# Performance work log

Hardware: AMD Instinct MI355X
Metric: run time of the kernel (lower is better)

The kernel has to match this reference:

```python
import jax, jax.numpy as jnp
import numpy as np

INV_SQRT2 = np.float32(2.0 ** -0.5)
EPS = 1e-5


def _bn5(x, g, b, m, v):
    # inference-mode BatchNorm3d over channel axis 1 of NCDHW
    r = (1, -1, 1, 1, 1)
    return (x - m.reshape(r)) * (g.reshape(r) * jax.lax.rsqrt(v.reshape(r) + EPS)) + b.reshape(r)


def _conv3d(x, w, b, dil=1, pad=0):
    out = jax.lax.conv_general_dilated(
        x, w, window_strides=(1, 1, 1), padding=[(pad, pad)] * 3,
        rhs_dilation=(dil, dil, dil),
        dimension_numbers=('NCDHW', 'OIDHW', 'NCDHW'))
    return out + b.reshape(1, -1, 1, 1, 1)


def _haar_dwt2(x):
    # pywt dwt2(x, 'haar', axes=(-3,-2)) for even-length axes.
    # axis -3 (D): a = approx, d = detail (pywt sign: (x0 - x1)/sqrt2)
    a = (x[:, :, 0::2] + x[:, :, 1::2]) * INV_SQRT2
    d = (x[:, :, 0::2] - x[:, :, 1::2]) * INV_SQRT2
    # axis -2 (H)
    LL = (a[:, :, :, 0::2] + a[:, :, :, 1::2]) * INV_SQRT2  # 'aa'
    HL = (a[:, :, :, 0::2] - a[:, :, :, 1::2]) * INV_SQRT2  # 'ad'
    LH = (d[:, :, :, 0::2] + d[:, :, :, 1::2]) * INV_SQRT2  # 'da'
    HH = (d[:, :, :, 0::2] - d[:, :, :, 1::2]) * INV_SQRT2  # 'dd'
    return LL, LH, HL, HH


def setup_inputs() -> dict:
    key = jax.random.key(0)
    ks = jax.random.split(key, 12)
    B, C1, D, H, W = 2, 60, 128, 128, 64
    CH, R = 64, 4  # gate channels, CH // reduction_ratio
    f32 = jnp.float32
    inp = {
        'x1': jax.random.normal(ks[0], (B, C1, D // 2, H // 2, W), f32),
        'x2': jax.random.normal(ks[1], (B, 1, D, H, W), f32),
        # BatchNorm3d(4) on dwt features
        'bn_g': jnp.ones(4, f32), 'bn_b': jnp.zeros(4, f32),
        'bn_m': jnp.zeros(4, f32), 'bn_v': jnp.ones(4, f32),
        # BAM channel gate: Linear(64->4), BN1d(4), Linear(4->64)
        'cg_w1': jax.random.normal(ks[2], (R, CH), f32) * 0.05,
        'cg_b1': jnp.zeros(R, f32),
        'cg_bng': jnp.ones(R, f32), 'cg_bnb': jnp.zeros(R, f32),
        'cg_bnm': jnp.zeros(R, f32), 'cg_bnv': jnp.ones(R, f32),
        'cg_w2': jax.random.normal(ks[3], (CH, R), f32) * 0.05,
        'cg_b2': jnp.zeros(CH, f32),
        # BAM spatial gate
        'sg_w0': jax.random.normal(ks[4], (R, CH, 1, 1, 1), f32) * 0.05,
        'sg_b0': jnp.zeros(R, f32),
        'sg_g0': jnp.ones(R, f32), 'sg_be0': jnp.zeros(R, f32),
        'sg_m0': jnp.zeros(R, f32), 'sg_v0': jnp.ones(R, f32),
        'sg_w1': jax.random.normal(ks[5], (R, R, 3, 3, 3), f32) * 0.05,
        'sg_b1': jnp.zeros(R, f32),
        'sg_g1': jnp.ones(R, f32), 'sg_be1': jnp.zeros(R, f32),
        'sg_m1': jnp.zeros(R, f32), 'sg_v1': jnp.ones(R, f32),
        'sg_w2': jax.random.normal(ks[6], (R, R, 3, 3, 3), f32) * 0.05,
        'sg_b2': jnp.zeros(R, f32),
        'sg_g2': jnp.ones(R, f32), 'sg_be2': jnp.zeros(R, f32),
        'sg_m2': jnp.zeros(R, f32), 'sg_v2': jnp.ones(R, f32),
        'sg_w3': jax.random.normal(ks[7], (1, R, 1, 1, 1), f32) * 0.05,
        'sg_b3': jnp.zeros(1, f32),
    }
    return inp


def reference(x1, x2, bn_g, bn_b, bn_m, bn_v,
              cg_w1, cg_b1, cg_bng, cg_bnb, cg_bnm, cg_bnv, cg_w2, cg_b2,
              sg_w0, sg_b0, sg_g0, sg_be0, sg_m0, sg_v0,
              sg_w1, sg_b1, sg_g1, sg_be1, sg_m1, sg_v1,
              sg_w2, sg_b2, sg_g2, sg_be2, sg_m2, sg_v2,
              sg_w3, sg_b3):
    LL, LH, HL, HH = _haar_dwt2(x2)
    dwt = jnp.concatenate([LL, LH, HL, HH], axis=1)          # [B,4,D/2,H/2,W]
    dwt = jax.nn.relu(_bn5(dwt, bn_g, bn_b, bn_m, bn_v))
    feat = jnp.concatenate([dwt, x1], axis=1)                # [B,64,D/2,H/2,W]

    # BAM channel gate
    pooled = feat.mean(axis=(2, 3, 4))                        # [B,64]
    h = pooled @ cg_w1.T + cg_b1
    h = jax.nn.relu((h - cg_bnm) * (cg_bng * jax.lax.rsqrt(cg_bnv + EPS)) + cg_bnb)
    att_c = (h @ cg_w2.T + cg_b2)[:, :, None, None, None]     # [B,64,1,1,1]

    # BAM spatial gate
    s = jax.nn.relu(_bn5(_conv3d(feat, sg_w0, sg_b0), sg_g0, sg_be0, sg_m0, sg_v0))
    s = jax.nn.relu(_bn5(_conv3d(s, sg_w1, sg_b1, dil=4, pad=4), sg_g1, sg_be1, sg_m1, sg_v1))
    s = jax.nn.relu(_bn5(_conv3d(s, sg_w2, sg_b2, dil=4, pad=4), sg_g2, sg_be2, sg_m2, sg_v2))
    att_s = _conv3d(s, sg_w3, sg_b3)                          # [B,1,D/2,H/2,W]

    scale = 1.0 + jax.nn.sigmoid(att_c + att_s)
    return (feat * scale, LL)
```

## Files before the change

### kernel.cpp

```cpp
#include <hip/hip_runtime.h>
#include <math.h>

#define EPSBN 1e-5f

constexpr int B   = 2;
constexpr int C1  = 60;
constexpr int NV  = 64 * 64 * 64;
constexpr int NB  = NV / 1024;

__global__ __launch_bounds__(256) void kA(
    const float* __restrict__ x1, const float* __restrict__ x2,
    const float* __restrict__ bn_g, const float* __restrict__ bn_b,
    const float* __restrict__ bn_m, const float* __restrict__ bn_v,
    const float* __restrict__ sg_w0, const float* __restrict__ sg_b0,
    const float* __restrict__ sg_g0, const float* __restrict__ sg_be0,
    const float* __restrict__ sg_m0, const float* __restrict__ sg_v0,
    float* __restrict__ dwt, float* __restrict__ s0,
    float* __restrict__ part, float* __restrict__ outLL)
{
    __shared__ float w0l[256];
    __shared__ float cA[4], cB[4];
    __shared__ float dsc[4], dsh[4];
    __shared__ float wsum[64][4];

    const int tid = threadIdx.x;
    w0l[tid] = sg_w0[tid];
    if (tid < 4) {
        float sc = sg_g0[tid] * rsqrtf(sg_v0[tid] + EPSBN);
        cA[tid] = sc;
        cB[tid] = (sg_b0[tid] - sg_m0[tid]) * sc + sg_be0[tid];
        float d = bn_g[tid] * rsqrtf(bn_v[tid] + EPSBN);
        dsc[tid] = d;
        dsh[tid] = bn_b[tid] - bn_m[tid] * d;
    }
    __syncthreads();

    const int b = blockIdx.y;
    const int v = blockIdx.x * 1024 + tid * 4;
    const int x = v & 63, y = (v >> 6) & 63, z = v >> 12;
    const int lane = tid & 63, wv = tid >> 6;

    const float* px2 = x2 + (size_t)b * (128 * 128 * 64);
    const size_t i00 = ((size_t)(2 * z) * 128 + 2 * y) * 64 + x;
    const float4 p00 = *(const float4*)(px2 + i00);
    const float4 p01 = *(const float4*)(px2 + i00 + 64);
    const float4 p10 = *(const float4*)(px2 + i00 + 8192);
    const float4 p11 = *(const float4*)(px2 + i00 + 8256);
    const float* q00 = (const float*)&p00; const float* q01 = (const float*)&p01;
    const float* q10 = (const float*)&p10; const float* q11 = (const float*)&p11;

    float tv[4][4];
    float llv[4];
    #pragma unroll
    for (int vi = 0; vi < 4; ++vi) {
        float a = q00[vi], bb = q01[vi], c = q10[vi], d = q11[vi];
        float LL = 0.5f * (a + bb + c + d);
        float LH = 0.5f * (a + bb - c - d);
        float HL = 0.5f * (a - bb + c - d);
        float HH = 0.5f * (a - bb - c + d);
        llv[vi] = LL;
        tv[vi][0] = fmaxf(LL * dsc[0] + dsh[0], 0.f);
        tv[vi][1] = fmaxf(LH * dsc[1] + dsh[1], 0.f);
        tv[vi][2] = fmaxf(HL * dsc[2] + dsh[2], 0.f);
        tv[vi][3] = fmaxf(HH * dsc[3] + dsh[3], 0.f);
    }
    *(float4*)(outLL + (size_t)b * NV + v) = make_float4(llv[0], llv[1], llv[2], llv[3]);

    float acc[4][4] = {};
    #pragma unroll
    for (int c = 0; c < 4; ++c) {
        #pragma unroll
        for (int vi = 0; vi < 4; ++vi) {
            float t = tv[vi][c];
            #pragma unroll
            for (int r = 0; r < 4; ++r) acc[vi][r] += w0l[r * 64 + c] * t;
        }
        float rs = tv[0][c] + tv[1][c] + tv[2][c] + tv[3][c];
        #pragma unroll
        for (int off = 32; off; off >>= 1) rs += __shfl_xor(rs, off);
        if (lane == 0) wsum[c][wv] = rs;
    }

    float4* pdwt = (float4*)dwt + (size_t)b * NV + v;
    #pragma unroll
    for (int vi = 0; vi < 4; ++vi)
        pdwt[vi] = make_float4(tv[vi][0], tv[vi][1], tv[vi][2], tv[vi][3]);

    const float* px1 = x1 + (size_t)b * C1 * NV + v;
    for (int c = 0; c < C1; ++c) {
        const float4 f = *(const float4*)(px1 + (size_t)c * NV);
        const float* fv = (const float*)&f;
        #pragma unroll
        for (int vi = 0; vi < 4; ++vi) {
            #pragma unroll
            for (int r = 0; r < 4; ++r) acc[vi][r] += w0l[r * 64 + 4 + c] * fv[vi];
        }
        float rs = f.x + f.y + f.z + f.w;
        #pragma unroll
        for (int off = 32; off; off >>= 1) rs += __shfl_xor(rs, off);
        if (lane == 0) wsum[4 + c][wv] = rs;
    }

    float4* ps0 = (float4*)s0 + (size_t)b * NV + v;
    #pragma unroll
    for (int vi = 0; vi < 4; ++vi)
        ps0[vi] = make_float4(fmaxf(acc[vi][0] * cA[0] + cB[0], 0.f),
                              fmaxf(acc[vi][1] * cA[1] + cB[1], 0.f),
                              fmaxf(acc[vi][2] * cA[2] + cB[2], 0.f),
                              fmaxf(acc[vi][3] * cA[3] + cB[3], 0.f));

    __syncthreads();
    if (tid < 64) {
        float p = wsum[tid][0] + wsum[tid][1] + wsum[tid][2] + wsum[tid][3];
        part[((size_t)b * 64 + tid) * NB + blockIdx.x] = p;
    }
}

__global__ __launch_bounds__(256) void kConv1(
    const float* __restrict__ sin_,
    const float* __restrict__ w, const float* __restrict__ bias,
    const float* __restrict__ g, const float* __restrict__ be,
    const float* __restrict__ m, const float* __restrict__ vv,
    float* __restrict__ outp)
{
    __shared__ float wl[432];
    __shared__ float cA[4], cB[4];
    const int tid = threadIdx.x;
    for (int i = tid; i < 432; i += 256) wl[i] = w[i];
    if (tid < 4) {
        float sc = g[tid] * rsqrtf(vv[tid] + EPSBN);
        cA[tid] = sc;
        cB[tid] = (bias[tid] - m[tid]) * sc + be[tid];
    }
    __syncthreads();

    const int b = blockIdx.y;
    const int v = blockIdx.x * 1024 + tid * 4;
    const int x = v & 63, y = (v >> 6) & 63, z = v >> 12;
    const float4* pin = (const float4*)sin_ + (size_t)b * NV;

    float acc[4][4] = {};
    #pragma unroll
    for (int kz = -1; kz <= 1; ++kz) {
        const int zz = z + 4 * kz;
        if ((unsigned)zz >= 64u) continue;
        #pragma unroll
        for (int ky = -1; ky <= 1; ++ky) {
            const int yy = y + 4 * ky;
            if ((unsigned)yy >= 64u) continue;
            #pragma unroll
            for (int kx = -1; kx <= 1; ++kx) {
                const int xx = x + 4 * kx;
                if ((unsigned)xx >= 64u) continue;
                const int t = (kz + 1) * 9 + (ky + 1) * 3 + (kx + 1);
                const int vt = zz * 4096 + yy * 64 + xx;
                #pragma unroll
                for (int vi = 0; vi < 4; ++vi) {
                    const float4 tap = pin[vt + vi];
                    acc[vi][0] += wl[      t] * tap.x + wl[ 27 + t] * tap.y + wl[ 54 + t] * tap.z + wl[ 81 + t] * tap.w;
                    acc[vi][1] += wl[108 + t] * tap.x + wl[135 + t] * tap.y + wl[162 + t] * tap.z + wl[189 + t] * tap.w;
                    acc[vi][2] += wl[216 + t] * tap.x + wl[243 + t] * tap.y + wl[270 + t] * tap.z + wl[297 + t] * tap.w;
                    acc[vi][3] += wl[324 + t] * tap.x + wl[351 + t] * tap.y + wl[378 + t] * tap.z + wl[405 + t] * tap.w;
                }
            }
        }
    }

    float4* po = (float4*)outp + (size_t)b * NV + v;
    #pragma unroll
    for (int vi = 0; vi < 4; ++vi)
        po[vi] = make_float4(fmaxf(acc[vi][0] * cA[0] + cB[0], 0.f),
                             fmaxf(acc[vi][1] * cA[1] + cB[1], 0.f),
                             fmaxf(acc[vi][2] * cA[2] + cB[2], 0.f),
                             fmaxf(acc[vi][3] * cA[3] + cB[3], 0.f));
}

__global__ __launch_bounds__(256) void kMLP(
    const float* __restrict__ part,
    const float* __restrict__ cg_w1, const float* __restrict__ cg_b1,
    const float* __restrict__ cg_bng, const float* __restrict__ cg_bnb,
    const float* __restrict__ cg_bnm, const float* __restrict__ cg_bnv,
    const float* __restrict__ cg_w2, const float* __restrict__ cg_b2,
    float* __restrict__ att_c)
{
    const int b = blockIdx.x;
    const int tid = threadIdx.x;
    __shared__ float pooled[64];
    __shared__ float h[4];

    const int c = tid >> 2, q = tid & 3;
    const float4* pp = (const float4*)(part + ((size_t)b * 64 + c) * NB + q * 64);
    float sm = 0.f;
    #pragma unroll
    for (int i = 0; i < 16; ++i) { float4 f = pp[i]; sm += f.x + f.y + f.z + f.w; }
    sm += __shfl_xor(sm, 1);
    sm += __shfl_xor(sm, 2);
    if (q == 0) pooled[c] = sm * (1.0f / NV);
    __syncthreads();
    if (tid < 4) {
        float a = cg_b1[tid];
        for (int cc = 0; cc < 64; ++cc) a += pooled[cc] * cg_w1[tid * 64 + cc];
        float sc = cg_bng[tid] * rsqrtf(cg_bnv[tid] + EPSBN);
        h[tid] = fmaxf((a - cg_bnm[tid]) * sc + cg_bnb[tid], 0.f);
    }
    __syncthreads();
    if (tid < 64) {
        float a = cg_b2[tid];
        #pragma unroll
        for (int r = 0; r < 4; ++r) a += h[r] * cg_w2[tid * 4 + r];
        att_c[b * 64 + tid] = a;
    }
}

__global__ __launch_bounds__(256) void kF(
    const float* __restrict__ x1,
    const float* __restrict__ dwt,
    const float* __restrict__ s1,
    const float* __restrict__ w, const float* __restrict__ bias,
    const float* __restrict__ g, const float* __restrict__ be,
    const float* __restrict__ m, const float* __restrict__ vv,
    const float* __restrict__ w3, const float* __restrict__ b3,
    const float* __restrict__ att_c,
    float* __restrict__ out0)
{
    __shared__ float wl[432];
    __shared__ float cA[4], cB[4], w3l[4], b3l;
    __shared__ float ec[64];
    const int tid = threadIdx.x;
    const int b = blockIdx.y;
    for (int i = tid; i < 432; i += 256) wl[i] = w[i];
    if (tid < 4) {
        float sc = g[tid] * rsqrtf(vv[tid] + EPSBN);
        cA[tid] = sc;
        cB[tid] = (bias[tid] - m[tid]) * sc + be[tid];
        w3l[tid] = w3[tid];
    }
    if (tid == 0) b3l = b3[0];
    if (tid < 64) ec[tid] = __expf(-att_c[b * 64 + tid]);
    __syncthreads();

    const int v = blockIdx.x * 1024 + tid * 4;
    const int x = v & 63, y = (v >> 6) & 63, z = v >> 12;
    const float4* pin = (const float4*)s1 + (size_t)b * NV;

    float acc[4][4] = {};
    #pragma unroll
    for (int kz = -1; kz <= 1; ++kz) {
        const int zz = z + 4 * kz;
        if ((unsigned)zz >= 64u) continue;
        #pragma unroll
        for (int ky = -1; ky <= 1; ++ky) {
            const int yy = y + 4 * ky;
            if ((unsigned)yy >= 64u) continue;
            #pragma unroll
            for (int kx = -1; kx <= 1; ++kx) {
                const int xx = x + 4 * kx;
                if ((unsigned)xx >= 64u) continue;
                const int t = (kz + 1) * 9 + (ky + 1) * 3 + (kx + 1);
                const int vt = zz * 4096 + yy * 64 + xx;
                #pragma unroll
                for (int vi = 0; vi < 4; ++vi) {
                    const float4 tap = pin[vt + vi];
                    acc[vi][0] += wl[      t] * tap.x + wl[ 27 + t] * tap.y + wl[ 54 + t] * tap.z + wl[ 81 + t] * tap.w;
                    acc[vi][1] += wl[108 + t] * tap.x + wl[135 + t] * tap.y + wl[162 + t] * tap.z + wl[189 + t] * tap.w;
                    acc[vi][2] += wl[216 + t] * tap.x + wl[243 + t] * tap.y + wl[270 + t] * tap.z + wl[297 + t] * tap.w;
                    acc[vi][3] += wl[324 + t] * tap.x + wl[351 + t] * tap.y + wl[378 + t] * tap.z + wl[405 + t] * tap.w;
                }
            }
        }
    }

    float eas[4];
    #pragma unroll
    for (int vi = 0; vi < 4; ++vi) {
        float r0 = fmaxf(acc[vi][0] * cA[0] + cB[0], 0.f);
        float r1 = fmaxf(acc[vi][1] * cA[1] + cB[1], 0.f);
        float r2 = fmaxf(acc[vi][2] * cA[2] + cB[2], 0.f);
        float r3 = fmaxf(acc[vi][3] * cA[3] + cB[3], 0.f);
        float as = b3l + w3l[0] * r0 + w3l[1] * r1 + w3l[2] * r2 + w3l[3] * r3;
        eas[vi] = __expf(-as);
    }

    float dv[4][4];
    const float4* pdwt = (const float4*)dwt + (size_t)b * NV + v;
    #pragma unroll
    for (int vi = 0; vi < 4; ++vi) {
        const float4 dq = pdwt[vi];
        dv[vi][0] = dq.x; dv[vi][1] = dq.y; dv[vi][2] = dq.z; dv[vi][3] = dq.w;
    }
    float* po = out0 + (size_t)b * 64 * NV + v;
    #pragma unroll
    for (int c = 0; c < 4; ++c) {
        float e = ec[c];
        float4 o;
        o.x = dv[0][c] * (1.f + __builtin_amdgcn_rcpf(1.f + e * eas[0]));
        o.y = dv[1][c] * (1.f + __builtin_amdgcn_rcpf(1.f + e * eas[1]));
        o.z = dv[2][c] * (1.f + __builtin_amdgcn_rcpf(1.f + e * eas[2]));
        o.w = dv[3][c] * (1.f + __builtin_amdgcn_rcpf(1.f + e * eas[3]));
        *(float4*)(po + (size_t)c * NV) = o;
    }
    const float* px1 = x1 + (size_t)b * C1 * NV + v;
    for (int c = 0; c < C1; ++c) {
        const float4 f = *(const float4*)(px1 + (size_t)c * NV);
        const float e = ec[4 + c];
        float4 o;
        o.x = f.x * (1.f + __builtin_amdgcn_rcpf(1.f + e * eas[0]));
        o.y = f.y * (1.f + __builtin_amdgcn_rcpf(1.f + e * eas[1]));
        o.z = f.z * (1.f + __builtin_amdgcn_rcpf(1.f + e * eas[2]));
        o.w = f.w * (1.f + __builtin_amdgcn_rcpf(1.f + e * eas[3]));
        *(float4*)(po + (size_t)(4 + c) * NV) = o;
    }
}

extern "C" void kernel_launch(void* const* d_in, const int* in_sizes, int n_in,
                              void* d_out, int out_size, void* d_ws, size_t ws_size,
                              hipStream_t stream)
{
    const float* x1 = (const float*)d_in[0];
    const float* x2 = (const float*)d_in[1];
    const float* bn_g = (const float*)d_in[2];
    const float* bn_b = (const float*)d_in[3];
    const float* bn_m = (const float*)d_in[4];
    const float* bn_v = (const float*)d_in[5];
    const float* cg_w1 = (const float*)d_in[6];
    const float* cg_b1 = (const float*)d_in[7];
    const float* cg_bng = (const float*)d_in[8];
    const float* cg_bnb = (const float*)d_in[9];
    const float* cg_bnm = (const float*)d_in[10];
    const float* cg_bnv = (const float*)d_in[11];
    const float* cg_w2 = (const float*)d_in[12];
    const float* cg_b2 = (const float*)d_in[13];
    const float* sg_w0 = (const float*)d_in[14];
    const float* sg_b0 = (const float*)d_in[15];
    const float* sg_g0 = (const float*)d_in[16];
    const float* sg_be0 = (const float*)d_in[17];
    const float* sg_m0 = (const float*)d_in[18];
    const float* sg_v0 = (const float*)d_in[19];
    const float* sg_w1 = (const float*)d_in[20];
    const float* sg_b1 = (const float*)d_in[21];
    const float* sg_g1 = (const float*)d_in[22];
    const float* sg_be1 = (const float*)d_in[23];
    const float* sg_m1 = (const float*)d_in[24];
    const float* sg_v1 = (const float*)d_in[25];
    const float* sg_w2 = (const float*)d_in[26];
    const float* sg_b2 = (const float*)d_in[27];
    const float* sg_g2 = (const float*)d_in[28];
    const float* sg_be2 = (const float*)d_in[29];
    const float* sg_m2 = (const float*)d_in[30];
    const float* sg_v2 = (const float*)d_in[31];
    const float* sg_w3 = (const float*)d_in[32];
    const float* sg_b3 = (const float*)d_in[33];

    float* ws = (float*)d_ws;
    float* dwt  = ws;
    float* s0   = ws + 2097152;
    float* s1   = ws + 4194304;
    float* part = ws + 6291456;
    float* attc = ws + 6324224;

    float* out0  = (float*)d_out;
    float* outLL = out0 + (size_t)B * 64 * NV;

    dim3 grid(NB, B), blk(256);
    kA<<<grid, blk, 0, stream>>>(x1, x2, bn_g, bn_b, bn_m, bn_v,
                                 sg_w0, sg_b0, sg_g0, sg_be0, sg_m0, sg_v0,
                                 dwt, s0, part, outLL);
    kConv1<<<grid, blk, 0, stream>>>(s0, sg_w1, sg_b1, sg_g1, sg_be1, sg_m1, sg_v1, s1);
    kMLP<<<dim3(B), blk, 0, stream>>>(part, cg_w1, cg_b1, cg_bng, cg_bnb, cg_bnm, cg_bnv,
                                      cg_w2, cg_b2, attc);
    kF<<<grid, blk, 0, stream>>>(x1, dwt, s1, sg_w2, sg_b2, sg_g2, sg_be2, sg_m2, sg_v2,
                                 sg_w3, sg_b3, attc, out0);
}
```

Measured before the change: 120.7 us.

## Halve per-thread work, fold channel MLP into conv1, split final gating into streaming kernel

Each thread now handles 2 voxels instead of 4, which doubles the grid of the stencil and pointwise kernels. The channel-gate MLP moves into an extra block of the first dilated conv, removing a separate launch. The dwt intermediate is stored channel-major. The last conv now writes a per-voxel exp(-att_s) map, and a new flat, fully coalesced multiply kernel applies the gate over all 64 channels. This aims for more parallelism and better-coalesced streaming in the final pass, at the cost of an extra round trip of the spatial-attention map through memory and one more launch.

```diff
diff --git a/kernel.cpp b/kernel.cpp
--- a/kernel.cpp
+++ b/kernel.cpp
@@ -6,7 +6,7 @@
 constexpr int B   = 2;
 constexpr int C1  = 60;
 constexpr int NV  = 64 * 64 * 64;
-constexpr int NB  = NV / 1024;
+constexpr int NBa = NV / 512;
 
 __global__ __launch_bounds__(256) void kA(
     const float* __restrict__ x1, const float* __restrict__ x2,
@@ -15,7 +15,7 @@
     const float* __restrict__ sg_w0, const float* __restrict__ sg_b0,
     const float* __restrict__ sg_g0, const float* __restrict__ sg_be0,
     const float* __restrict__ sg_m0, const float* __restrict__ sg_v0,
-    float* __restrict__ dwt, float* __restrict__ s0,
+    float* __restrict__ dwtM, float* __restrict__ s0,
     float* __restrict__ part, float* __restrict__ outLL)
 {
     __shared__ float w0l[256];
@@ -36,23 +36,22 @@
     __syncthreads();
 
     const int b = blockIdx.y;
-    const int v = blockIdx.x * 1024 + tid * 4;
+    const int v = blockIdx.x * 512 + tid * 2;
     const int x = v & 63, y = (v >> 6) & 63, z = v >> 12;
     const int lane = tid & 63, wv = tid >> 6;
 
     const float* px2 = x2 + (size_t)b * (128 * 128 * 64);
     const size_t i00 = ((size_t)(2 * z) * 128 + 2 * y) * 64 + x;
-    const float4 p00 = *(const float4*)(px2 + i00);
-    const float4 p01 = *(const float4*)(px2 + i00 + 64);
-    const float4 p10 = *(const float4*)(px2 + i00 + 8192);
-    const float4 p11 = *(const float4*)(px2 + i00 + 8256);
+    const float2 p00 = *(const float2*)(px2 + i00);
+    const float2 p01 = *(const float2*)(px2 + i00 + 64);
+    const float2 p10 = *(const float2*)(px2 + i00 + 8192);
+    const float2 p11 = *(const float2*)(px2 + i00 + 8256);
     const float* q00 = (const float*)&p00; const float* q01 = (const float*)&p01;
     const float* q10 = (const float*)&p10; const float* q11 = (const float*)&p11;
 
-    float tv[4][4];
-    float llv[4];
-    #pragma unroll
-    for (int vi = 0; vi < 4; ++vi) {
+    float tv[2][4], llv[2];
+    #pragma unroll
+    for (int vi = 0; vi < 2; ++vi) {
         float a = q00[vi], bb = q01[vi], c = q10[vi], d = q11[vi];
         float LL = 0.5f * (a + bb + c + d);
         float LH = 0.5f * (a + bb - c - d);
@@ -64,38 +63,33 @@
         tv[vi][2] = fmaxf(HL * dsc[2] + dsh[2], 0.f);
         tv[vi][3] = fmaxf(HH * dsc[3] + dsh[3], 0.f);
     }
-    *(float4*)(outLL + (size_t)b * NV + v) = make_float4(llv[0], llv[1], llv[2], llv[3]);
-
-    float acc[4][4] = {};
+    *(float2*)(outLL + (size_t)b * NV + v) = make_float2(llv[0], llv[1]);
+
+    float acc[2][4] = {};
     #pragma unroll
     for (int c = 0; c < 4; ++c) {
         #pragma unroll
-        for (int vi = 0; vi < 4; ++vi) {
+        for (int vi = 0; vi < 2; ++vi) {
             float t = tv[vi][c];
             #pragma unroll
             for (int r = 0; r < 4; ++r) acc[vi][r] += w0l[r * 64 + c] * t;
         }
-        float rs = tv[0][c] + tv[1][c] + tv[2][c] + tv[3][c];
+        float rs = tv[0][c] + tv[1][c];
         #pragma unroll
         for (int off = 32; off; off >>= 1) rs += __shfl_xor(rs, off);
         if (lane == 0) wsum[c][wv] = rs;
-    }
-
-    float4* pdwt = (float4*)dwt + (size_t)b * NV + v;
-    #pragma unroll
-    for (int vi = 0; vi < 4; ++vi)
-        pdwt[vi] = make_float4(tv[vi][0], tv[vi][1], tv[vi][2], tv[vi][3]);
+        *(float2*)(dwtM + ((size_t)b * 4 + c) * NV + v) = make_float2(tv[0][c], tv[1][c]);
+    }
 
     const float* px1 = x1 + (size_t)b * C1 * NV + v;
     for (int c = 0; c < C1; ++c) {
-        const float4 f = *(const float4*)(px1 + (size_t)c * NV);
-        const float* fv = (const float*)&f;
-        #pragma unroll
-        for (int vi = 0; vi < 4; ++vi) {
-            #pragma unroll
-            for (int r = 0; r < 4; ++r) acc[vi][r] += w0l[r * 64 + 4 + c] * fv[vi];
-        }
-        float rs = f.x + f.y + f.z + f.w;
+        const float2 f = *(const float2*)(px1 + (size_t)c * NV);
+        #pragma unroll
+        for (int r = 0; r < 4; ++r) {
+            acc[0][r] += w0l[r * 64 + 4 + c] * f.x;
+            acc[1][r] += w0l[r * 64 + 4 + c] * f.y;
+        }
+        float rs = f.x + f.y;
         #pragma unroll
         for (int off = 32; off; off >>= 1) rs += __shfl_xor(rs, off);
         if (lane == 0) wsum[4 + c][wv] = rs;
@@ -103,7 +97,7 @@
 
     float4* ps0 = (float4*)s0 + (size_t)b * NV + v;
     #pragma unroll
-    for (int vi = 0; vi < 4; ++vi)
+    for (int vi = 0; vi < 2; ++vi)
         ps0[vi] = make_float4(fmaxf(acc[vi][0] * cA[0] + cB[0], 0.f),
                               fmaxf(acc[vi][1] * cA[1] + cB[1], 0.f),
                               fmaxf(acc[vi][2] * cA[2] + cB[2], 0.f),
@@ -112,7 +106,7 @@
     __syncthreads();
     if (tid < 64) {
         float p = wsum[tid][0] + wsum[tid][1] + wsum[tid][2] + wsum[tid][3];
-        part[((size_t)b * 64 + tid) * NB + blockIdx.x] = p;
+        part[((size_t)b * 64 + tid) * NBa + blockIdx.x] = p;
     }
 }
 
@@ -121,11 +115,47 @@
     const float* __restrict__ w, const float* __restrict__ bias,
     const float* __restrict__ g, const float* __restrict__ be,
     const float* __restrict__ m, const float* __restrict__ vv,
+    const float* __restrict__ part,
+    const float* __restrict__ cg_w1, const float* __restrict__ cg_b1,
+    const float* __restrict__ cg_bng, const float* __restrict__ cg_bnb,
+    const float* __restrict__ cg_bnm, const float* __restrict__ cg_bnv,
+    const float* __restrict__ cg_w2, const float* __restrict__ cg_b2,
+    float* __restrict__ ec,
     float* __restrict__ outp)
 {
+    const int tid = threadIdx.x;
+    const int b = blockIdx.y;
+
+    if (blockIdx.x == NBa) {
+        __shared__ float pooled[64];
+        __shared__ float h[4];
+        const int c = tid >> 2, q = tid & 3;
+        const float4* pp = (const float4*)(part + ((size_t)b * 64 + c) * NBa + q * 128);
+        float sm = 0.f;
+        #pragma unroll
+        for (int i = 0; i < 32; ++i) { float4 f = pp[i]; sm += f.x + f.y + f.z + f.w; }
+        sm += __shfl_xor(sm, 1);
+        sm += __shfl_xor(sm, 2);
+        if (q == 0) pooled[c] = sm * (1.0f / NV);
+        __syncthreads();
+        if (tid < 4) {
+            float a = cg_b1[tid];
+            for (int cc = 0; cc < 64; ++cc) a += pooled[cc] * cg_w1[tid * 64 + cc];
+            float sc = cg_bng[tid] * rsqrtf(cg_bnv[tid] + EPSBN);
+            h[tid] = fmaxf((a - cg_bnm[tid]) * sc + cg_bnb[tid], 0.f);
+        }
+        __syncthreads();
+        if (tid < 64) {
+            float a = cg_b2[tid];
+            #pragma unroll
+            for (int r = 0; r < 4; ++r) a += h[r] * cg_w2[tid * 4 + r];
+            ec[b * 64 + tid] = __expf(-a);
+        }
+        return;
+    }
+
     __shared__ float wl[432];
     __shared__ float cA[4], cB[4];
-    const int tid = threadIdx.x;
     for (int i = tid; i < 432; i += 256) wl[i] = w[i];
     if (tid < 4) {
         float sc = g[tid] * rsqrtf(vv[tid] + EPSBN);
@@ -134,12 +164,11 @@
     }
     __syncthreads();
 
-    const int b = blockIdx.y;
-    const int v = blockIdx.x * 1024 + tid * 4;
+    const int v = blockIdx.x * 512 + tid * 2;
     const int x = v & 63, y = (v >> 6) & 63, z = v >> 12;
     const float4* pin = (const float4*)sin_ + (size_t)b * NV;
 
-    float acc[4][4] = {};
+    float acc[2][4] = {};
     #pragma unroll
     for (int kz = -1; kz <= 1; ++kz) {
         const int zz = z + 4 * kz;
@@ -155,7 +184,7 @@
                 const int t = (kz + 1) * 9 + (ky + 1) * 3 + (kx + 1);
                 const int vt = zz * 4096 + yy * 64 + xx;
                 #pragma unroll
-                for (int vi = 0; vi < 4; ++vi) {
+                for (int vi = 0; vi < 2; ++vi) {
                     const float4 tap = pin[vt + vi];
                     acc[vi][0] += wl[      t] * tap.x + wl[ 27 + t] * tap.y + wl[ 54 + t] * tap.z + wl[ 81 + t] * tap.w;
                     acc[vi][1] += wl[108 + t] * tap.x + wl[135 + t] * tap.y + wl[162 + t] * tap.z + wl[189 + t] * tap.w;
@@ -168,66 +197,24 @@
 
     float4* po = (float4*)outp + (size_t)b * NV + v;
     #pragma unroll
-    for (int vi = 0; vi < 4; ++vi)
+    for (int vi = 0; vi < 2; ++vi)
         po[vi] = make_float4(fmaxf(acc[vi][0] * cA[0] + cB[0], 0.f),
                              fmaxf(acc[vi][1] * cA[1] + cB[1], 0.f),
                              fmaxf(acc[vi][2] * cA[2] + cB[2], 0.f),
                              fmaxf(acc[vi][3] * cA[3] + cB[3], 0.f));
 }
 
-__global__ __launch_bounds__(256) void kMLP(
-    const float* __restrict__ part,
-    const float* __restrict__ cg_w1, const float* __restrict__ cg_b1,
-    const float* __restrict__ cg_bng, const float* __restrict__ cg_bnb,
-    const float* __restrict__ cg_bnm, const float* __restrict__ cg_bnv,
-    const float* __restrict__ cg_w2, const float* __restrict__ cg_b2,
-    float* __restrict__ att_c)
-{
-    const int b = blockIdx.x;
-    const int tid = threadIdx.x;
-    __shared__ float pooled[64];
-    __shared__ float h[4];
-
-    const int c = tid >> 2, q = tid & 3;
-    const float4* pp = (const float4*)(part + ((size_t)b * 64 + c) * NB + q * 64);
-    float sm = 0.f;
-    #pragma unroll
-    for (int i = 0; i < 16; ++i) { float4 f = pp[i]; sm += f.x + f.y + f.z + f.w; }
-    sm += __shfl_xor(sm, 1);
-    sm += __shfl_xor(sm, 2);
-    if (q == 0) pooled[c] = sm * (1.0f / NV);
-    __syncthreads();
-    if (tid < 4) {
-        float a = cg_b1[tid];
-        for (int cc = 0; cc < 64; ++cc) a += pooled[cc] * cg_w1[tid * 64 + cc];
-        float sc = cg_bng[tid] * rsqrtf(cg_bnv[tid] + EPSBN);
-        h[tid] = fmaxf((a - cg_bnm[tid]) * sc + cg_bnb[tid], 0.f);
-    }
-    __syncthreads();
-    if (tid < 64) {
-        float a = cg_b2[tid];
-        #pragma unroll
-        for (int r = 0; r < 4; ++r) a += h[r] * cg_w2[tid * 4 + r];
-        att_c[b * 64 + tid] = a;
-    }
-}
-
-__global__ __launch_bounds__(256) void kF(
-    const float* __restrict__ x1,
-    const float* __restrict__ dwt,
-    const float* __restrict__ s1,
+__global__ __launch_bounds__(256) void kConv2(
+    const float* __restrict__ sin_,
     const float* __restrict__ w, const float* __restrict__ bias,
     const float* __restrict__ g, const float* __restrict__ be,
     const float* __restrict__ m, const float* __restrict__ vv,
     const float* __restrict__ w3, const float* __restrict__ b3,
-    const float* __restrict__ att_c,
-    float* __restrict__ out0)
+    float* __restrict__ es)
 {
     __shared__ float wl[432];
     __shared__ float cA[4], cB[4], w3l[4], b3l;
-    __shared__ float ec[64];
     const int tid = threadIdx.x;
-    const int b = blockIdx.y;
     for (int i = tid; i < 432; i += 256) wl[i] = w[i];
     if (tid < 4) {
         float sc = g[tid] * rsqrtf(vv[tid] + EPSBN);
@@ -236,14 +223,14 @@
         w3l[tid] = w3[tid];
     }
     if (tid == 0) b3l = b3[0];
-    if (tid < 64) ec[tid] = __expf(-att_c[b * 64 + tid]);
     __syncthreads();
 
-    const int v = blockIdx.x * 1024 + tid * 4;
+    const int b = blockIdx.y;
+    const int v = blockIdx.x * 512 + tid * 2;
     const int x = v & 63, y = (v >> 6) & 63, z = v >> 12;
-    const float4* pin = (const float4*)s1 + (size_t)b * NV;
-
-    float acc[4][4] = {};
+    const float4* pin = (const float4*)sin_ + (size_t)b * NV;
+
+    float acc[2][4] = {};
     #pragma unroll
     for (int kz = -1; kz <= 1; ++kz) {
         const int zz = z + 4 * kz;
@@ -259,7 +246,7 @@
                 const int t = (kz + 1) * 9 + (ky + 1) * 3 + (kx + 1);
                 const int vt = zz * 4096 + yy * 64 + xx;
                 #pragma unroll
-                for (int vi = 0; vi < 4; ++vi) {
+                for (int vi = 0; vi < 2; ++vi) {
                     const float4 tap = pin[vt + vi];
                     acc[vi][0] += wl[      t] * tap.x + wl[ 27 + t] * tap.y + wl[ 54 + t] * tap.z + wl[ 81 + t] * tap.w;
                     acc[vi][1] += wl[108 + t] * tap.x + wl[135 + t] * tap.y + wl[162 + t] * tap.z + wl[189 + t] * tap.w;
@@ -270,45 +257,45 @@
         }
     }
 
-    float eas[4];
-    #pragma unroll
-    for (int vi = 0; vi < 4; ++vi) {
+    float ev[2];
+    #pragma unroll
+    for (int vi = 0; vi < 2; ++vi) {
         float r0 = fmaxf(acc[vi][0] * cA[0] + cB[0], 0.f);
         float r1 = fmaxf(acc[vi][1] * cA[1] + cB[1], 0.f);
         float r2 = fmaxf(acc[vi][2] * cA[2] + cB[2], 0.f);
         float r3 = fmaxf(acc[vi][3] * cA[3] + cB[3], 0.f);
-        float as = b3l + w3l[0] * r0 + w3l[1] * r1 + w3l[2] * r2 + w3l[3] * r3;
-        eas[vi] = __expf(-as);
-    }
-
-    float dv[4][4];
-    const float4* pdwt = (const float4*)dwt + (size_t)b * NV + v;
-    #pragma unroll
-    for (int vi = 0; vi < 4; ++vi) {
-        const float4 dq = pdwt[vi];
-        dv[vi][0] = dq.x; dv[vi][1] = dq.y; dv[vi][2] = dq.z; dv[vi][3] = dq.w;
-    }
-    float* po = out0 + (size_t)b * 64 * NV + v;
-    #pragma unroll
-    for (int c = 0; c < 4; ++c) {
-        float e = ec[c];
+        ev[vi] = __expf(-(b3l + w3l[0] * r0 + w3l[1] * r1 + w3l[2] * r2 + w3l[3] * r3));
+    }
+    *(float2*)(es + (size_t)b * NV + v) = make_float2(ev[0], ev[1]);
+}
+
+__global__ __launch_bounds__(256) void kMul(
+    const float* __restrict__ x1,
+    const float* __restrict__ dwtM,
+    const float* __restrict__ es,
+    const float* __restrict__ ec,
+    float* __restrict__ out0)
+{
+    const int i0 = blockIdx.x * 256 + threadIdx.x;
+    #pragma unroll 4
+    for (int it = 0; it < 16; ++it) {
+        const size_t idx = (size_t)i0 + (size_t)it * 524288;
+        const int b  = (int)(idx >> 22);
+        const int r  = (int)(idx & 4194303);
+        const int c  = r >> 16;
+        const int vq = r & 65535;
+        const float* base = (c < 4)
+            ? dwtM + ((size_t)b * 4 + c) * NV
+            : x1   + ((size_t)b * C1 + (c - 4)) * NV;
+        const float4 in4 = *(const float4*)(base + (size_t)vq * 4);
+        const float4 es4 = ((const float4*)(es + (size_t)b * NV))[vq];
+        const float  e   = ec[(b << 6) + c];
         float4 o;
-        o.x = dv[0][c] * (1.f + __builtin_amdgcn_rcpf(1.f + e * eas[0]));
-        o.y = dv[1][c] * (1.f + __builtin_amdgcn_rcpf(1.f + e * eas[1]));
-        o.z = dv[2][c] * (1.f + __builtin_amdgcn_rcpf(1.f + e * eas[2]));
-        o.w = dv[3][c] * (1.f + __builtin_amdgcn_rcpf(1.f + e * eas[3]));
-        *(float4*)(po + (size_t)c * NV) = o;
-    }
-    const float* px1 = x1 + (size_t)b * C1 * NV + v;
-    for (int c = 0; c < C1; ++c) {
-        const float4 f = *(const float4*)(px1 + (size_t)c * NV);
-        const float e = ec[4 + c];
-        float4 o;
-        o.x = f.x * (1.f + __builtin_amdgcn_rcpf(1.f + e * eas[0]));
-        o.y = f.y * (1.f + __builtin_amdgcn_rcpf(1.f + e * eas[1]));
-        o.z = f.z * (1.f + __builtin_amdgcn_rcpf(1.f + e * eas[2]));
-        o.w = f.w * (1.f + __builtin_amdgcn_rcpf(1.f + e * eas[3]));
-        *(float4*)(po + (size_t)(4 + c) * NV) = o;
+        o.x = in4.x * (1.f + __builtin_amdgcn_rcpf(1.f + e * es4.x));
+        o.y = in4.y * (1.f + __builtin_amdgcn_rcpf(1.f + e * es4.y));
+        o.z = in4.z * (1.f + __builtin_amdgcn_rcpf(1.f + e * es4.z));
+        o.w = in4.w * (1.f + __builtin_amdgcn_rcpf(1.f + e * es4.w));
+        ((float4*)out0)[idx] = o;
     }
 }
 
@@ -352,22 +339,24 @@
     const float* sg_b3 = (const float*)d_in[33];
 
     float* ws = (float*)d_ws;
-    float* dwt  = ws;
+    float* dwtM = ws;
     float* s0   = ws + 2097152;
     float* s1   = ws + 4194304;
-    float* part = ws + 6291456;
-    float* attc = ws + 6324224;
+    float* es   = ws + 6291456;
+    float* part = ws + 6815744;
+    float* ec   = ws + 6881280;
 
     float* out0  = (float*)d_out;
     float* outLL = out0 + (size_t)B * 64 * NV;
 
-    dim3 grid(NB, B), blk(256);
-    kA<<<grid, blk, 0, stream>>>(x1, x2, bn_g, bn_b, bn_m, bn_v,
-                                 sg_w0, sg_b0, sg_g0, sg_be0, sg_m0, sg_v0,
-                                 dwt, s0, part, outLL);
-    kConv1<<<grid, blk, 0, stream>>>(s0, sg_w1, sg_b1, sg_g1, sg_be1, sg_m1, sg_v1, s1);
-    kMLP<<<dim3(B), blk, 0, stream>>>(part, cg_w1, cg_b1, cg_bng, cg_bnb, cg_bnm, cg_bnv,
-                                      cg_w2, cg_b2, attc);
-    kF<<<grid, blk, 0, stream>>>(x1, dwt, s1, sg_w2, sg_b2, sg_g2, sg_be2, sg_m2, sg_v2,
-                                 sg_w3, sg_b3, attc, out0);
-}
+    dim3 blk(256);
+    kA<<<dim3(NBa, B), blk, 0, stream>>>(x1, x2, bn_g, bn_b, bn_m, bn_v,
+                                         sg_w0, sg_b0, sg_g0, sg_be0, sg_m0, sg_v0,
+                                         dwtM, s0, part, outLL);
+    kConv1<<<dim3(NBa + 1, B), blk, 0, stream>>>(s0, sg_w1, sg_b1, sg_g1, sg_be1, sg_m1, sg_v1,
+                                                 part, cg_w1, cg_b1, cg_bng, cg_bnb, cg_bnm, cg_bnv,
+                                                 cg_w2, cg_b2, ec, s1);
+    kConv2<<<dim3(NBa, B), blk, 0, stream>>>(s1, sg_w2, sg_b2, sg_g2, sg_be2, sg_m2, sg_v2,
+                                             sg_w3, sg_b3, es);
+    kMul<<<dim3(2048), blk, 0, stream>>>(x1, dwtM, es, ec, out0);
+}
```

Result: faster. 118.0 us (-2.2%).
